# Performance work log

Measured on AMD Instinct MI355X. Metric: run time of the kernel, lower is better.

The kernel has to match this reference:

```python
import jax, jax.numpy as jnp
import numpy as np

DIM = 2048
ATT_DIM = 2048
N_HEADS = 16
HEAD_DIM = ATT_DIM // N_HEADS  # 128


def setup_inputs() -> dict:
    key = jax.random.key(0)
    k1, k2, k3 = jax.random.split(key, 3)
    tgt_len = 2048
    x = jax.random.normal(k1, (tgt_len, DIM), dtype=jnp.float32)
    # nn.Linear weights: [out_features, in_features], no bias
    w_in = jax.random.normal(k2, (3 * ATT_DIM, DIM), dtype=jnp.float32) * (1.0 / np.sqrt(DIM))
    w_out = jax.random.normal(k3, (DIM, ATT_DIM), dtype=jnp.float32) * (1.0 / np.sqrt(ATT_DIM))
    return {"x": x, "w_in": w_in, "w_out": w_out, "tgt_len": tgt_len}


def reference(x, w_in, w_out, tgt_len):
    # qkv projection: Linear -> x @ W^T, then split into thirds
    qkv = x @ w_in.T                      # [T, 3*att_dim]
    q, k, v = jnp.split(qkv, 3, axis=-1)  # each [T, att_dim]
    # [T, H, Dh] -> [H, T, Dh]
    q = q.reshape(tgt_len, N_HEADS, HEAD_DIM).transpose(1, 0, 2)
    k = k.reshape(tgt_len, N_HEADS, HEAD_DIM).transpose(1, 0, 2)
    v = v.reshape(tgt_len, N_HEADS, HEAD_DIM).transpose(1, 0, 2)
    scaling = 1.0 / jnp.sqrt(jnp.asarray(HEAD_DIM, dtype=x.dtype))
    scores = jnp.einsum("htd,hsd->hts", q, k) * scaling  # [H, T, T]
    attn = jax.nn.softmax(scores, axis=-1)
    ctx = jnp.einsum("hts,hsd->htd", attn, v)             # [H, T, Dh]
    ctx = ctx.transpose(1, 0, 2).reshape(tgt_len, ATT_DIM)
    return ctx @ w_out.T                                   # [T, dim]
```

## Files before the change

kernel.cpp:

```cpp
#include <hip/hip_runtime.h>

#define T_LEN 2048
#define DIM 2048
#define NH 16
#define HD 128
#define QKV_LD 6144

typedef __attribute__((ext_vector_type(8))) short short8;
typedef __attribute__((ext_vector_type(4))) short short4v;
typedef __attribute__((ext_vector_type(4))) float f32x4;
typedef __attribute__((ext_vector_type(4))) float float4v;
typedef __attribute__((ext_vector_type(4))) unsigned short ushort4v;
typedef __attribute__((ext_vector_type(2))) unsigned int uint2v;

static __device__ __forceinline__ unsigned short f2bf(float f) {
  unsigned u = __builtin_bit_cast(unsigned, f);
  u += 0x7fffu + ((u >> 16) & 1u);
  return (unsigned short)(u >> 16);
}

static __device__ __forceinline__ unsigned cvtpk_bf16(float lo, float hi) {
  unsigned r;
  asm("v_cvt_pk_bf16_f32 %0, %1, %2" : "=v"(r) : "v"(lo), "v"(hi));
  return r;
}

static __device__ __forceinline__ float max3f(float a, float b, float c) {
  return fmaxf(fmaxf(a, b), c);
}

static __device__ __forceinline__ f32x4 mfma16(short8 a, short8 b, f32x4 c) {
  return __builtin_amdgcn_mfma_f32_16x16x32_bf16(a, b, c, 0, 0, 0);
}

#define GLDS16(SRC, DST)                                                            \
  __builtin_amdgcn_global_load_lds((__attribute__((address_space(1))) void*)(SRC),  \
                                   (__attribute__((address_space(3))) void*)(DST),  \
                                   16, 0, 0)

__global__ void cast3_f32_bf16(const float* __restrict__ a, unsigned short* __restrict__ oa, int na4,
                               const float* __restrict__ b, unsigned short* __restrict__ ob, int nb4,
                               const float* __restrict__ c, unsigned short* __restrict__ oc, int nc4) {
  const int stride = gridDim.x * blockDim.x;
  const int g = blockIdx.x * blockDim.x + threadIdx.x;
#define CAST_LOOP(SRC, DST, N4)                                  \
  for (int i = g; i < (N4); i += stride) {                       \
    float4v f = ((const float4v*)(SRC))[i];                      \
    ushort4v o;                                                  \
    o.x = f2bf(f.x); o.y = f2bf(f.y);                            \
    o.z = f2bf(f.z); o.w = f2bf(f.w);                            \
    ((ushort4v*)(DST))[i] = o;                                   \
  }
  CAST_LOOP(a, oa, na4)
  CAST_LOOP(b, ob, nb4)
  CAST_LOOP(c, oc, nc4)
#undef CAST_LOOP
}

template <int MODE>
__global__ __launch_bounds__(256) void gemm_bt_128(
    const unsigned short* __restrict__ A,
    const unsigned short* __restrict__ B,
    void* __restrict__ Cv, unsigned short* __restrict__ vt,
    int M, int N, int K) {
  __shared__ unsigned short As[128 * 64];
  __shared__ unsigned short Bs[128 * 64];
  const int tid = threadIdx.x;
  const int wave = tid >> 6;
  const int lane = tid & 63;
  const int l15 = lane & 15, l16 = lane >> 4;
  const int bm = blockIdx.y * 128;
  const int bn = blockIdx.x * 128;
  const int wr = wave >> 1, wc = wave & 1;

  f32x4 acc[4][4] = {};

  int srow[4], scol[4];
#pragma unroll
  for (int i = 0; i < 4; ++i) {
    int lin = i * 4096 + tid * 16;
    int row = lin >> 7;
    int cb = lin & 127;
    srow[i] = row;
    scol[i] = (cb ^ ((row & 7) << 4)) >> 1;
  }

  for (int k0 = 0; k0 < K; k0 += 64) {
#pragma unroll
    for (int i = 0; i < 4; ++i) {
      GLDS16(A + (size_t)(bm + srow[i]) * K + k0 + scol[i], As + i * 2048 + wave * 512);
      GLDS16(B + (size_t)(bn + srow[i]) * K + k0 + scol[i], Bs + i * 2048 + wave * 512);
    }
    __syncthreads();
#pragma unroll
    for (int kk = 0; kk < 2; ++kk) {
      const int cb = kk * 64 + l16 * 16;
      short8 af[4], bfr[4];
#pragma unroll
      for (int m = 0; m < 4; ++m) {
        int row = wr * 64 + m * 16 + l15;
        af[m] = *(const short8*)((const char*)As + row * 128 + (cb ^ ((row & 7) << 4)));
      }
#pragma unroll
      for (int n = 0; n < 4; ++n) {
        int row = wc * 64 + n * 16 + l15;
        bfr[n] = *(const short8*)((const char*)Bs + row * 128 + (cb ^ ((row & 7) << 4)));
      }
#pragma unroll
      for (int m = 0; m < 4; ++m)
#pragma unroll
        for (int n = 0; n < 4; ++n)
          acc[m][n] = mfma16(af[m], bfr[n], acc[m][n]);
    }
    __syncthreads();
  }

  const bool vthird = (MODE == 2) && (bn >= 2 * DIM);
#pragma unroll
  for (int m = 0; m < 4; ++m)
#pragma unroll
    for (int n = 0; n < 4; ++n) {
      int row = bm + wr * 64 + m * 16 + l16 * 4;
      int col = bn + wc * 64 + n * 16 + l15;
      if (MODE == 2 && vthird) {
        short4v w;
#pragma unroll
        for (int j = 0; j < 4; ++j) w[j] = (short)f2bf(acc[m][n][j]);
        *(short4v*)(vt + (size_t)(col - 2 * DIM) * T_LEN + row) = w;
      } else {
#pragma unroll
        for (int j = 0; j < 4; ++j) {
          if (MODE == 0)
            ((float*)Cv)[(size_t)(row + j) * N + col] = acc[m][n][j];
          else
            ((unsigned short*)Cv)[(size_t)(row + j) * N + col] = f2bf(acc[m][n][j]);
        }
      }
    }
}

__global__ __launch_bounds__(256) void gemm_bt_12864(
    const unsigned short* __restrict__ A,
    const unsigned short* __restrict__ B,
    float* __restrict__ C, int M, int N, int K) {
  __shared__ unsigned short As[128 * 64];
  __shared__ unsigned short Bs[64 * 64];
  const int tid = threadIdx.x;
  const int wave = tid >> 6;
  const int lane = tid & 63;
  const int l15 = lane & 15, l16 = lane >> 4;
  const int bm = blockIdx.y * 128;
  const int bn = blockIdx.x * 64;
  const int wr = wave >> 1, wc = wave & 1;

  f32x4 acc[4][2] = {};

  int srow[4], scol[4];
#pragma unroll
  for (int i = 0; i < 4; ++i) {
    int lin = i * 4096 + tid * 16;
    int row = lin >> 7;
    int cb = lin & 127;
    srow[i] = row;
    scol[i] = (cb ^ ((row & 7) << 4)) >> 1;
  }

  for (int k0 = 0; k0 < K; k0 += 64) {
#pragma unroll
    for (int i = 0; i < 4; ++i)
      GLDS16(A + (size_t)(bm + srow[i]) * K + k0 + scol[i], As + i * 2048 + wave * 512);
#pragma unroll
    for (int i = 0; i < 2; ++i)
      GLDS16(B + (size_t)(bn + srow[i]) * K + k0 + scol[i], Bs + i * 2048 + wave * 512);
    __syncthreads();
#pragma unroll
    for (int kk = 0; kk < 2; ++kk) {
      const int cb = kk * 64 + l16 * 16;
      short8 af[4], bfr[2];
#pragma unroll
      for (int m = 0; m < 4; ++m) {
        int row = wr * 64 + m * 16 + l15;
        af[m] = *(const short8*)((const char*)As + row * 128 + (cb ^ ((row & 7) << 4)));
      }
#pragma unroll
      for (int n = 0; n < 2; ++n) {
        int row = wc * 32 + n * 16 + l15;
        bfr[n] = *(const short8*)((const char*)Bs + row * 128 + (cb ^ ((row & 7) << 4)));
      }
#pragma unroll
      for (int m = 0; m < 4; ++m)
#pragma unroll
        for (int n = 0; n < 2; ++n)
          acc[m][n] = mfma16(af[m], bfr[n], acc[m][n]);
    }
    __syncthreads();
  }

#pragma unroll
  for (int m = 0; m < 4; ++m)
#pragma unroll
    for (int n = 0; n < 2; ++n) {
      int row = bm + wr * 64 + m * 16 + l16 * 4;
      int col = bn + wc * 32 + n * 16 + l15;
#pragma unroll
      for (int j = 0; j < 4; ++j)
        C[(size_t)(row + j) * N + col] = acc[m][n][j];
    }
}

__global__ __launch_bounds__(256) void attn_fwd(
    const unsigned short* __restrict__ qkv,
    const unsigned short* __restrict__ vt,
    unsigned short* __restrict__ ctx) {
  __shared__ char lds[73728];
  const int tid = threadIdx.x;
  const int wave = tid >> 6;
  const int lane = tid & 63;
  const int l15 = lane & 15, l16 = lane >> 4;
  const int h = blockIdx.y;
  const int q0 = blockIdx.x * 64 + wave * 16;
  const float SCL = 0.08838834764831845f * 1.4426950408889634f;

  short8 qf[4];
#pragma unroll
  for (int kk = 0; kk < 4; ++kk)
    qf[kk] = *(const short8*)(qkv + (size_t)(q0 + l15) * QKV_LD + h * HD + kk * 32 + l16 * 8);

  f32x4 acc_o[8] = {};
  float m_r = -1e30f;
  float l_r = 0.f;

  const int xm = (l15 & 7) << 4;
  const char* krd0 = lds + 8192 + l15 * 256 + ((l16 * 16) ^ xm);
  const char* krd1 = lds + 8192 + l15 * 256 + ((64 + l16 * 16) ^ xm);
  const char* vrd0 = lds + 40960 + l15 * 128 + ((l16 * 16) ^ xm);
  const char* vrd1 = lds + 40960 + l15 * 128 + ((64 + l16 * 16) ^ xm);
  char* pwr0 = lds + wave * 2048 + ((l15 * 128 + 0 * 32 + l16 * 8) ^ xm);
  char* pwr1 = lds + wave * 2048 + ((l15 * 128 + 1 * 32 + l16 * 8) ^ xm);
  char* pwr2 = lds + wave * 2048 + ((l15 * 128 + 2 * 32 + l16 * 8) ^ xm);
  char* pwr3 = lds + wave * 2048 + ((l15 * 128 + 3 * 32 + l16 * 8) ^ xm);
  const char* prd0 = lds + wave * 2048 + l15 * 128 + ((l16 * 16) ^ xm);
  const char* prd1 = lds + wave * 2048 + l15 * 128 + ((64 + l16 * 16) ^ xm);
  char* kdst = lds + 8192 + wave * 1024;
  char* vdst = lds + 40960 + wave * 1024;

  const unsigned short* kp[4];
  const unsigned short* vp[4];
#pragma unroll
  for (int i = 0; i < 4; ++i) {
    int lin = i * 4096 + tid * 16;
    int r = lin >> 8;
    int cb = lin & 255;
    kp[i] = qkv + 2048 + h * HD + (size_t)r * QKV_LD + ((cb ^ ((r & 7) << 4)) >> 1);
    r = lin >> 7;
    cb = lin & 127;
    vp[i] = vt + (size_t)h * HD * T_LEN + (size_t)r * T_LEN + ((cb ^ ((r & 7) << 4)) >> 1);
  }

#define STAGE_KV(BUFOFF)                                                               \
  do {                                                                                 \
    _Pragma("unroll")                                                                  \
    for (int i = 0; i < 4; ++i) {                                                      \
      GLDS16(kp[i], kdst + (BUFOFF) + i * 4096);                                       \
      GLDS16(vp[i], vdst + (BUFOFF) + i * 4096);                                       \
      kp[i] += 64 * QKV_LD;                                                            \
      vp[i] += 64;                                                                     \
    }                                                                                  \
  } while (0)

#define COMPUTE(BUFOFF)                                                                \
  do {                                                                                 \
                     \
    f32x4 st[4] = {};                                                                  \
    _Pragma("unroll")                                                                  \
    for (int c = 0; c < 4; ++c) {                                                      \
      st[c] = mfma16(*(const short8*)(krd0 + (BUFOFF) + c * 4096), qf[0], st[c]);      \
      st[c] = mfma16(*(const short8*)(krd1 + (BUFOFF) + c * 4096), qf[1], st[c]);      \
      st[c] = mfma16(*(const short8*)(krd0 + (BUFOFF) + 128 + c * 4096), qf[2], st[c]);\
      st[c] = mfma16(*(const short8*)(krd1 + (BUFOFF) + 128 + c * 4096), qf[3], st[c]);\
    }                                                                                  \
                                         \
    float ma = max3f(st[0][0], st[0][1], st[0][2]);                                    \
    float mb = max3f(st[0][3], st[1][0], st[1][1]);                                    \
    float mc = max3f(st[1][2], st[1][3], st[2][0]);                                    \
    float md = max3f(st[2][1], st[2][2], st[2][3]);                                    \
    float me = max3f(st[3][0], st[3][1], st[3][2]);                                    \
    float pmax = fmaxf(max3f(ma, mb, mc), max3f(md, me, st[3][3])) * SCL;              \
    pmax = fmaxf(pmax, __shfl_xor(pmax, 16));                                          \
    pmax = fmaxf(pmax, __shfl_xor(pmax, 32));                                          \
    if (!__all(pmax - m_r <= 8.0f)) {                                                  \
      float nm = fmaxf(m_r, pmax);                                                     \
      float corr = __builtin_amdgcn_exp2f(m_r - nm);                                   \
      m_r = nm;                                                                        \
      l_r *= corr;                                                                     \
      float cj[4];                                                                     \
      _Pragma("unroll")                                                                \
      for (int j = 0; j < 4; ++j) cj[j] = __shfl(corr, l16 * 4 + j);                   \
      _Pragma("unroll")                                                                \
      for (int d = 0; d < 8; ++d)                                                      \
        _Pragma("unroll")                                                              \
        for (int j = 0; j < 4; ++j) acc_o[d][j] *= cj[j];                              \
    }                                                                                  \
    float p[4][4];                                                                     \
    _Pragma("unroll")                                                                  \
    for (int c = 0; c < 4; ++c)                                                        \
      _Pragma("unroll")                                                                \
      for (int j = 0; j < 4; ++j)                                                      \
        p[c][j] = __builtin_amdgcn_exp2f(st[c][j] * SCL - m_r);                        \
    float s01 = (p[0][0] + p[0][1]) + (p[0][2] + p[0][3]);                             \
    float s23 = (p[1][0] + p[1][1]) + (p[1][2] + p[1][3]);                             \
    float s45 = (p[2][0] + p[2][1]) + (p[2][2] + p[2][3]);                             \
    float s67 = (p[3][0] + p[3][1]) + (p[3][2] + p[3][3]);                             \
    float tsum = (s01 + s23) + (s45 + s67);                                            \
    tsum += __shfl_xor(tsum, 16);                                                      \
    tsum += __shfl_xor(tsum, 32);                                                      \
    l_r += tsum;                                                                       \
                  \
    {                                                                                  \
      uint2v w;                                                                        \
      w.x = cvtpk_bf16(p[0][0], p[0][1]); w.y = cvtpk_bf16(p[0][2], p[0][3]);          \
      *(uint2v*)pwr0 = w;                                                              \
      w.x = cvtpk_bf16(p[1][0], p[1][1]); w.y = cvtpk_bf16(p[1][2], p[1][3]);          \
      *(uint2v*)pwr1 = w;                                                              \
      w.x = cvtpk_bf16(p[2][0], p[2][1]); w.y = cvtpk_bf16(p[2][2], p[2][3]);          \
      *(uint2v*)pwr2 = w;                                                              \
      w.x = cvtpk_bf16(p[3][0], p[3][1]); w.y = cvtpk_bf16(p[3][2], p[3][3]);          \
      *(uint2v*)pwr3 = w;                                                              \
    }                                                                                  \
                                                                     \
    {                                                                                  \
      short8 pa0 = *(const short8*)prd0;                                               \
      short8 pa1 = *(const short8*)prd1;                                               \
      _Pragma("unroll")                                                                \
      for (int d = 0; d < 8; ++d) {                                                    \
        acc_o[d] = mfma16(pa0, *(const short8*)(vrd0 + (BUFOFF) + d * 2048), acc_o[d]);\
        acc_o[d] = mfma16(pa1, *(const short8*)(vrd1 + (BUFOFF) + d * 2048), acc_o[d]);\
      }                                                                                \
    }                                                                                  \
  } while (0)

  STAGE_KV(0);
  __syncthreads();

  for (int i = 0; i < 16; ++i) {
    STAGE_KV(16384);
    COMPUTE(0);
    __syncthreads();
    if (i < 15) STAGE_KV(0);
    COMPUTE(16384);
    __syncthreads();
  }
#undef STAGE_KV
#undef COMPUTE

  float lq[4];
#pragma unroll
  for (int j = 0; j < 4; ++j) lq[j] = 1.0f / __shfl(l_r, l16 * 4 + j);
#pragma unroll
  for (int d = 0; d < 8; ++d)
#pragma unroll
    for (int j = 0; j < 4; ++j) {
      int row = q0 + l16 * 4 + j;
      int col = h * HD + d * 16 + l15;
      ctx[(size_t)row * DIM + col] = f2bf(acc_o[d][j] * lq[j]);
    }
}

extern "C" void kernel_launch(void* const* d_in, const int* in_sizes, int n_in,
                              void* d_out, int out_size, void* d_ws, size_t ws_size,
                              hipStream_t stream) {
  const float* x = (const float*)d_in[0];
  const float* w_in = (const float*)d_in[1];
  const float* w_out = (const float*)d_in[2];

  char* ws = (char*)d_ws;
  unsigned short* xbf  = (unsigned short*)(ws + 0);
  unsigned short* wibf = (unsigned short*)(ws + 8388608);
  unsigned short* wobf = (unsigned short*)(ws + 33554432);
  unsigned short* qkv  = (unsigned short*)(ws + 41943040);
  unsigned short* ctx  = (unsigned short*)(ws + 67108864);
  unsigned short* vt   = (unsigned short*)(ws + 75497472);

  cast3_f32_bf16<<<2048, 256, 0, stream>>>(
      x, xbf, (T_LEN * DIM) / 4,
      w_in, wibf, (3 * DIM * DIM) / 4,
      w_out, wobf, (DIM * DIM) / 4);

  gemm_bt_128<2><<<dim3(48, 16), 256, 0, stream>>>(
      xbf, wibf, (void*)qkv, vt, T_LEN, 3 * DIM, DIM);
  attn_fwd<<<dim3(32, 16), 256, 0, stream>>>(qkv, vt, ctx);
  gemm_bt_12864<<<dim3(32, 16), 256, 0, stream>>>(ctx, wobf, (float*)d_out, T_LEN, DIM, DIM);
}
```

Measured before the change: 169.5 us.

## Software-pipeline attention: overlap next tile QK^T with current softmax and PV

```diff
diff --git a/kernel.cpp b/kernel.cpp
--- a/kernel.cpp
+++ b/kernel.cpp
@@ -227,6 +227,7 @@
     qf[kk] = *(const short8*)(qkv + (size_t)(q0 + l15) * QKV_LD + h * HD + kk * 32 + l16 * 8);
 
   f32x4 acc_o[8] = {};
+  f32x4 stc[4], stp[4];
   float m_r = -1e30f;
   float l_r = 0.f;
 
@@ -257,35 +258,44 @@
     vp[i] = vt + (size_t)h * HD * T_LEN + (size_t)r * T_LEN + ((cb ^ ((r & 7) << 4)) >> 1);
   }
 
-#define STAGE_KV(BUFOFF)                                                               \
+#define STAGE_K(BUFOFF)                                                                \
   do {                                                                                 \
     _Pragma("unroll")                                                                  \
     for (int i = 0; i < 4; ++i) {                                                      \
       GLDS16(kp[i], kdst + (BUFOFF) + i * 4096);                                       \
+      kp[i] += 64 * QKV_LD;                                                            \
+    }                                                                                  \
+  } while (0)
+
+#define STAGE_V(BUFOFF)                                                                \
+  do {                                                                                 \
+    _Pragma("unroll")                                                                  \
+    for (int i = 0; i < 4; ++i) {                                                      \
       GLDS16(vp[i], vdst + (BUFOFF) + i * 4096);                                       \
-      kp[i] += 64 * QKV_LD;                                                            \
       vp[i] += 64;                                                                     \
     }                                                                                  \
   } while (0)
 
-#define COMPUTE(BUFOFF)                                                                \
+#define QKT(BUFOFF)                                                                    \
   do {                                                                                 \
-                     \
-    f32x4 st[4] = {};                                                                  \
     _Pragma("unroll")                                                                  \
     for (int c = 0; c < 4; ++c) {                                                      \
-      st[c] = mfma16(*(const short8*)(krd0 + (BUFOFF) + c * 4096), qf[0], st[c]);      \
-      st[c] = mfma16(*(const short8*)(krd1 + (BUFOFF) + c * 4096), qf[1], st[c]);      \
-      st[c] = mfma16(*(const short8*)(krd0 + (BUFOFF) + 128 + c * 4096), qf[2], st[c]);\
-      st[c] = mfma16(*(const short8*)(krd1 + (BUFOFF) + 128 + c * 4096), qf[3], st[c]);\
-    }                                                                                  \
-                                         \
-    float ma = max3f(st[0][0], st[0][1], st[0][2]);                                    \
-    float mb = max3f(st[0][3], st[1][0], st[1][1]);                                    \
-    float mc = max3f(st[1][2], st[1][3], st[2][0]);                                    \
-    float md = max3f(st[2][1], st[2][2], st[2][3]);                                    \
-    float me = max3f(st[3][0], st[3][1], st[3][2]);                                    \
-    float pmax = fmaxf(max3f(ma, mb, mc), max3f(md, me, st[3][3])) * SCL;              \
+      stc[c] = f32x4{0.f, 0.f, 0.f, 0.f};                                              \
+      stc[c] = mfma16(*(const short8*)(krd0 + (BUFOFF) + c * 4096), qf[0], stc[c]);    \
+      stc[c] = mfma16(*(const short8*)(krd1 + (BUFOFF) + c * 4096), qf[1], stc[c]);    \
+      stc[c] = mfma16(*(const short8*)(krd0 + (BUFOFF) + 128 + c * 4096), qf[2], stc[c]); \
+      stc[c] = mfma16(*(const short8*)(krd1 + (BUFOFF) + 128 + c * 4096), qf[3], stc[c]); \
+    }                                                                                  \
+  } while (0)
+
+#define SMPV(VOFF)                                                                     \
+  do {                                                                                 \
+    float ma = max3f(stp[0][0], stp[0][1], stp[0][2]);                                 \
+    float mb = max3f(stp[0][3], stp[1][0], stp[1][1]);                                 \
+    float mc = max3f(stp[1][2], stp[1][3], stp[2][0]);                                 \
+    float md = max3f(stp[2][1], stp[2][2], stp[2][3]);                                 \
+    float me = max3f(stp[3][0], stp[3][1], stp[3][2]);                                 \
+    float pmax = fmaxf(max3f(ma, mb, mc), max3f(md, me, stp[3][3])) * SCL;             \
     pmax = fmaxf(pmax, __shfl_xor(pmax, 16));                                          \
     pmax = fmaxf(pmax, __shfl_xor(pmax, 32));                                          \
     if (!__all(pmax - m_r <= 8.0f)) {                                                  \
@@ -306,7 +316,7 @@
     for (int c = 0; c < 4; ++c)                                                        \
       _Pragma("unroll")                                                                \
       for (int j = 0; j < 4; ++j)                                                      \
-        p[c][j] = __builtin_amdgcn_exp2f(st[c][j] * SCL - m_r);                        \
+        p[c][j] = __builtin_amdgcn_exp2f(stp[c][j] * SCL - m_r);                       \
     float s01 = (p[0][0] + p[0][1]) + (p[0][2] + p[0][3]);                             \
     float s23 = (p[1][0] + p[1][1]) + (p[1][2] + p[1][3]);                             \
     float s45 = (p[2][0] + p[2][1]) + (p[2][2] + p[2][3]);                             \
@@ -315,7 +325,6 @@
     tsum += __shfl_xor(tsum, 16);                                                      \
     tsum += __shfl_xor(tsum, 32);                                                      \
     l_r += tsum;                                                                       \
-                  \
     {                                                                                  \
       uint2v w;                                                                        \
       w.x = cvtpk_bf16(p[0][0], p[0][1]); w.y = cvtpk_bf16(p[0][2], p[0][3]);          \
@@ -327,31 +336,60 @@
       w.x = cvtpk_bf16(p[3][0], p[3][1]); w.y = cvtpk_bf16(p[3][2], p[3][3]);          \
       *(uint2v*)pwr3 = w;                                                              \
     }                                                                                  \
-                                                                     \
     {                                                                                  \
       short8 pa0 = *(const short8*)prd0;                                               \
       short8 pa1 = *(const short8*)prd1;                                               \
       _Pragma("unroll")                                                                \
       for (int d = 0; d < 8; ++d) {                                                    \
-        acc_o[d] = mfma16(pa0, *(const short8*)(vrd0 + (BUFOFF) + d * 2048), acc_o[d]);\
-        acc_o[d] = mfma16(pa1, *(const short8*)(vrd1 + (BUFOFF) + d * 2048), acc_o[d]);\
+        acc_o[d] = mfma16(pa0, *(const short8*)(vrd0 + (VOFF) + d * 2048), acc_o[d]);  \
+        acc_o[d] = mfma16(pa1, *(const short8*)(vrd1 + (VOFF) + d * 2048), acc_o[d]);  \
       }                                                                                \
     }                                                                                  \
   } while (0)
 
-  STAGE_KV(0);
+#define COPY_ST()                                                                      \
+  do {                                                                                 \
+    _Pragma("unroll")                                                                  \
+    for (int c = 0; c < 4; ++c) stp[c] = stc[c];                                       \
+  } while (0)
+
+  STAGE_K(0);
   __syncthreads();
 
-  for (int i = 0; i < 16; ++i) {
-    STAGE_KV(16384);
-    COMPUTE(0);
-    __syncthreads();
-    if (i < 15) STAGE_KV(0);
-    COMPUTE(16384);
-    __syncthreads();
-  }
-#undef STAGE_KV
-#undef COMPUTE
+  STAGE_K(16384);
+  STAGE_V(0);
+  QKT(0);
+  COPY_ST();
+  __syncthreads();
+
+  STAGE_K(0);
+  STAGE_V(16384);
+  QKT(16384);
+  SMPV(0);
+  COPY_ST();
+  __syncthreads();
+
+  for (int i = 1; i < 16; ++i) {
+    STAGE_K(16384);
+    STAGE_V(0);
+    QKT(0);
+    SMPV(16384);
+    COPY_ST();
+    __syncthreads();
+    if (i < 15) STAGE_K(0);
+    STAGE_V(16384);
+    QKT(16384);
+    SMPV(0);
+    COPY_ST();
+    __syncthreads();
+  }
+
+  SMPV(16384);
+#undef STAGE_K
+#undef STAGE_V
+#undef QKT
+#undef SMPV
+#undef COPY_ST
 
   float lq[4];
 #pragma unroll
```

Measured after the change: 168.7 us. No clear change (-0.5%).
